# Performance work log

Hardware: AMD Instinct MI355X
Metric: run time of the kernel (lower is better)

Reference implementation:

```python
import jax, jax.numpy as jnp
import numpy as np

MAXLEN = 100  # target_node_incoming_edge_maxlim in to_dense_batch_JY


def setup_inputs() -> dict:
    key = jax.random.key(0)
    ks = jax.random.split(key, 6)
    N, F, H, B = 500000, 64, 64, 8192
    x = jax.random.normal(ks[0], (N, F), dtype=jnp.float32)
    index = jnp.sort(jax.random.randint(ks[1], (N,), 0, B)).astype(jnp.int64)
    s = 1.0 / np.sqrt(H)  # torch LSTM reset_parameters: U(-1/sqrt(H), 1/sqrt(H))
    W_ih = jax.random.uniform(ks[2], (4 * H, F), jnp.float32, -s, s)
    W_hh = jax.random.uniform(ks[3], (4 * H, H), jnp.float32, -s, s)
    b_ih = jax.random.uniform(ks[4], (4 * H,), jnp.float32, -s, s)
    b_hh = jax.random.uniform(ks[5], (4 * H,), jnp.float32, -s, s)
    return {"x": x, "W_ih": W_ih, "W_hh": W_hh, "b_ih": b_ih, "b_hh": b_hh,
            "index": index, "dim_size": B}


def _lstm_last_hidden(dense, mask, W_ih, W_hh, b_ih, b_hh):
    """Run a single-layer LSTM over dense [B,L,F]; freeze state where mask is
    False, which reproduces pack_sequence semantics (ht = hidden at last valid
    step of each sequence; zero-length sequences stay at h0=0)."""
    B, L, F = dense.shape
    H = W_hh.shape[1]
    # input projection for all timesteps at once: [B, L, 4H]
    xg = jnp.einsum('blf,gf->blg', dense, W_ih) + (b_ih + b_hh)

    def step(carry, inp):
        h, c = carry
        g_x, m = inp                      # g_x: [B,4H], m: [B] bool
        g = g_x + h @ W_hh.T
        i, f, gc, o = jnp.split(g, 4, axis=-1)  # torch gate order: i, f, g, o
        i = jax.nn.sigmoid(i)
        f = jax.nn.sigmoid(f)
        gc = jnp.tanh(gc)
        o = jax.nn.sigmoid(o)
        c_new = f * c + i * gc
        h_new = o * jnp.tanh(c_new)
        m2 = m[:, None]
        return (jnp.where(m2, h_new, h), jnp.where(m2, c_new, c)), None

    h0 = jnp.zeros((B, H), dense.dtype)
    (h, _c), _ = jax.lax.scan(step, (h0, h0),
                              (jnp.swapaxes(xg, 0, 1), mask.T))
    return h  # [B, H] == ht[-1]


def reference(x, W_ih, W_hh, b_ih, b_hh, index, dim_size):
    N, F = x.shape
    index = index.astype(jnp.int32)
    # per-graph node counts and exclusive-cumsum offsets (index is sorted)
    counts = jax.ops.segment_sum(jnp.ones(N, jnp.int32), index,
                                 num_segments=dim_size)
    offsets = jnp.concatenate([jnp.zeros(1, jnp.int32),
                               jnp.cumsum(counts)[:-1].astype(jnp.int32)])
    pos = jnp.arange(N, dtype=jnp.int32) - offsets[index]  # position in graph
    valid = pos < MAXLEN                                   # truncate to 100
    # scatter into dense [B, MAXLEN, F]; invalid rows are zeroed and added at
    # slot 0 so they are no-ops
    dense = jnp.zeros((dim_size, MAXLEN, F), x.dtype)
    dense = dense.at[index, jnp.where(valid, pos, 0)].add(
        jnp.where(valid[:, None], x, 0.0))
    seq_len = jnp.minimum(counts, MAXLEN)
    mask = jnp.arange(MAXLEN)[None, :] < seq_len[:, None]  # [B, MAXLEN]
    return _lstm_last_hidden(dense, mask, W_ih, W_hh, b_ih, b_hh)
```

## Files before the change

kernel.cpp:

```cpp
#include <hip/hip_runtime.h>

#define MAXLEN 100
#define HDIM 64
#define CH 4
#define NSEG 12
#define SROW 72
#define SPLANE (CH * SROW + 8)
#define HSTR 72
#define L2E 1.44269504f

typedef __attribute__((ext_vector_type(8))) short bf16x8;
typedef __attribute__((ext_vector_type(4))) float f32x4;

#define LGKM_BARRIER() asm volatile("s_waitcnt lgkmcnt(0)\n\ts_barrier" ::: "memory")

__device__ __forceinline__ unsigned short f2bf_u(float f) {
    unsigned u = __float_as_uint(f);
    u += 0x7fffu + ((u >> 16) & 1u);
    return (unsigned short)(u >> 16);
}
__device__ __forceinline__ unsigned pk2(float a, float b) {
    return (unsigned)f2bf_u(a) | ((unsigned)f2bf_u(b) << 16);
}
__device__ __forceinline__ bf16x8 pack8(f32x4 a, f32x4 b) {
    union { unsigned u[4]; bf16x8 v; } c;
    c.u[0] = pk2(a[0], a[1]); c.u[1] = pk2(a[2], a[3]);
    c.u[2] = pk2(b[0], b[1]); c.u[3] = pk2(b[2], b[3]);
    return c.v;
}
__device__ __forceinline__ float sig_b(float v, float bs) {
    return __builtin_amdgcn_rcpf(1.0f + __builtin_amdgcn_exp2f(fmaf(v, -L2E, bs)));
}
__device__ __forceinline__ float tanh_b(float v, float bs2) {
    return fmaf(2.0f, __builtin_amdgcn_rcpf(1.0f + __builtin_amdgcn_exp2f(fmaf(v, -2.0f * L2E, bs2))), -1.0f);
}
__device__ __forceinline__ float tanh_p(float v) {
    return fmaf(2.0f, __builtin_amdgcn_rcpf(1.0f + __builtin_amdgcn_exp2f(v * (-2.0f * L2E))), -1.0f);
}

__global__ __launch_bounds__(256, 3)
void lstm12_kernel(const float* __restrict__ x,
                   const float* __restrict__ Wih,
                   const float* __restrict__ Whh,
                   const float* __restrict__ bih,
                   const float* __restrict__ bhh,
                   const int* __restrict__ index,
                   float* __restrict__ out, int N, int B) {
    const int tid  = threadIdx.x;
    const int w    = tid >> 6;
    const int lane = tid & 63;
    const int l15  = lane & 15;
    const int quad = lane >> 4;
    const int segbase = blockIdx.x * NSEG;
    const int ncol = w * 16 + l15;

    __shared__ __align__(16) unsigned short xst[NSEG * SPLANE];
    __shared__ __align__(16) unsigned short hst[2][16][HSTR];
    __shared__ int sstart[NSEG], slen[NSEG];

    if (tid < NSEG) {
        const int b = segbase + tid;
        int s = 0, len = 0;
        if (b < B) {
            int lo = 0, hi = N;
            while (lo < hi) { int m = (lo + hi) >> 1; if (index[m] < b) lo = m + 1; else hi = m; }
            s = lo;
            hi = N;
            while (lo < hi) { int m = (lo + hi) >> 1; if (index[m] < b + 1) lo = m + 1; else hi = m; }
            len = lo - s;
            len = len < MAXLEN ? len : MAXLEN;
        }
        sstart[tid] = s;
        slen[tid] = len;
    }
    for (int i = tid; i < 2 * 16 * HSTR / 2; i += 256) ((int*)hst)[i] = 0;
    __syncthreads();

    bf16x8 wi[4][2], wh[4][2];
    float bs[4];
#pragma unroll
    for (int g = 0; g < 4; ++g) {
        const int row = g * HDIM + ncol;
        const float bb = bih[row] + bhh[row];
        bs[g] = (g == 2) ? (-2.0f * L2E) * bb : (-L2E) * bb;
#pragma unroll
        for (int kt = 0; kt < 2; ++kt) {
            const f32x4* pi = (const f32x4*)(Wih + (size_t)row * HDIM + kt * 32 + quad * 8);
            const f32x4* ph = (const f32x4*)(Whh + (size_t)row * HDIM + kt * 32 + quad * 8);
            wi[g][kt] = pack8(pi[0], pi[1]);
            wh[g][kt] = pack8(ph[0], ph[1]);
        }
    }

    int len3[3];
#pragma unroll
    for (int r = 0; r < 3; ++r) len3[r] = slen[quad * 3 + r];
    int lmax = 0;
#pragma unroll
    for (int i = 0; i < NSEG; ++i) { int v = slen[i]; lmax = v > lmax ? v : lmax; }
    lmax = __builtin_amdgcn_readfirstlane(lmax);

    const int sS = tid >> 4, sT = (tid >> 2) & 3, sC = tid & 3;
    const int sst = (tid < 192) ? sstart[sS] : 0;
    const int sln = (tid < 192) ? slen[sS] : 0;

    f32x4 pre[4];

#define ISSUE(t0_)                                                              \
    if (w < 3) {                                                                \
        int ct = (t0_) + sT;                                                    \
        ct = (sln > 0) ? (ct < sln ? ct : sln - 1) : 0;                         \
        int row = sst + ct;                                                     \
        row = row < N - 1 ? row : N - 1;                                        \
        const f32x4* p_ = (const f32x4*)(x + (size_t)row * HDIM + sC * 16);     \
        pre[0] = p_[0]; pre[1] = p_[1]; pre[2] = p_[2]; pre[3] = p_[3];         \
    }
#define COMMIT()                                                                \
    if (w < 3) {                                                                \
        uint4 o1, o2;                                                           \
        o1.x = pk2(pre[0][0], pre[0][1]); o1.y = pk2(pre[0][2], pre[0][3]);     \
        o1.z = pk2(pre[1][0], pre[1][1]); o1.w = pk2(pre[1][2], pre[1][3]);     \
        o2.x = pk2(pre[2][0], pre[2][1]); o2.y = pk2(pre[2][2], pre[2][3]);     \
        o2.z = pk2(pre[3][0], pre[3][1]); o2.w = pk2(pre[3][2], pre[3][3]);     \
        unsigned short* d_ = &xst[sS * SPLANE + sT * SROW + sC * 16];           \
        *(uint4*)d_ = o1; *(uint4*)(d_ + 8) = o2;                               \
    }

    const int m3 = l15 & 3;
    const int xp = (l15 >> 2) * 3 + (m3 < 2 ? m3 : 2);
    const unsigned short* xb = &xst[xp * SPLANE + quad * 8];

    f32x4 accx[4];
#define ACCX(tt_)                                                               \
    {                                                                           \
        const unsigned short* xr_ = xb + (tt_) * SROW;                          \
        bf16x8 xa0_ = *(const bf16x8*)(xr_);                                    \
        bf16x8 xa1_ = *(const bf16x8*)(xr_ + 32);                               \
        _Pragma("unroll")                                                       \
        for (int g_ = 0; g_ < 4; ++g_) {                                        \
            f32x4 a_ = __builtin_amdgcn_mfma_f32_16x16x32_bf16(xa0_, wi[g_][0], cz, 0, 0, 0); \
            accx[g_] = __builtin_amdgcn_mfma_f32_16x16x32_bf16(xa1_, wi[g_][1], a_, 0, 0, 0); \
        }                                                                       \
    }

    float c3[3] = {0, 0, 0}, h3[3] = {0, 0, 0};
    const f32x4 cz = {0.0f, 0.0f, 0.0f, 0.0f};
    const int nch = (lmax + CH - 1) / CH;

    if (nch > 0) {
        ISSUE(0);
        COMMIT();
        LGKM_BARRIER();
        ACCX(0);
        if (nch > 1) ISSUE(CH);

        for (int ch = 0; ch < nch; ++ch) {
            const int t0 = ch * CH;
#pragma unroll
            for (int tt = 0; tt < CH; ++tt) {
                const int t = t0 + tt;
                const int pb = tt & 1, nb = pb ^ 1;

                const unsigned short* hr = &hst[pb][l15][quad * 8];
                bf16x8 ha0 = *(const bf16x8*)(hr);
                bf16x8 ha1 = *(const bf16x8*)(hr + 32);

                f32x4 acc[4];
#pragma unroll
                for (int g = 0; g < 4; ++g) {
                    f32x4 a = __builtin_amdgcn_mfma_f32_16x16x32_bf16(ha0, wh[g][0], accx[g], 0, 0, 0);
                    acc[g] = __builtin_amdgcn_mfma_f32_16x16x32_bf16(ha1, wh[g][1], a, 0, 0, 0);
                }

                if (tt + 1 < CH) ACCX(tt + 1);

#pragma unroll
                for (int r = 0; r < 3; ++r) {
                    float gi = sig_b (acc[0][r], bs[0]);
                    float gf = sig_b (acc[1][r], bs[1]);
                    float gg = tanh_b(acc[2][r], bs[2]);
                    float go = sig_b (acc[3][r], bs[3]);
                    float cn = fmaf(gf, c3[r], gi * gg);
                    float hn = go * tanh_p(cn);
                    const bool up = t < len3[r];
                    c3[r] = up ? cn : c3[r];
                    h3[r] = up ? hn : h3[r];
                    hst[nb][quad * 4 + r][ncol] = f2bf_u(h3[r]);
                }
                LGKM_BARRIER();
            }
            if (ch + 1 < nch) {
                COMMIT();
                LGKM_BARRIER();
                ACCX(0);
                if (ch + 2 < nch) ISSUE((ch + 2) * CH);
            }
        }
    }

#pragma unroll
    for (int r = 0; r < 3; ++r) {
        const int seg = segbase + quad * 3 + r;
        if (seg < B) out[(size_t)seg * HDIM + ncol] = h3[r];
    }
#undef ISSUE
#undef COMMIT
#undef ACCX
}

extern "C" void kernel_launch(void* const* d_in, const int* in_sizes, int n_in,
                              void* d_out, int out_size, void* d_ws, size_t ws_size,
                              hipStream_t stream) {
    const float* x     = (const float*)d_in[0];
    const float* Wih   = (const float*)d_in[1];
    const float* Whh   = (const float*)d_in[2];
    const float* bih   = (const float*)d_in[3];
    const float* bhh   = (const float*)d_in[4];
    const int*   index = (const int*)d_in[5];

    const int N = in_sizes[5];
    const int B = out_size / HDIM;

    const int nblocks = (B + NSEG - 1) / NSEG;
    lstm12_kernel<<<nblocks, 256, 0, stream>>>(x, Wih, Whh, bih, bhh, index,
                                               (float*)d_out, N, B);
}
```

Measured before the change: 251.5 us.

## Sort segments by length into blocks to balance LSTM recurrence work

Adds two pre-kernels: one computes segment start offsets from the sorted index, and one counting-sorts segments by truncated length into slots. The LSTM kernel then handles groups of 12 similar-length segments per block, so each block's step count matches its members and lanes do not idle waiting on the longest sequence. This costs two extra launches, including a single-block sort, plus an indirection when writing outputs. It falls back to the old per-block binary search when the workspace is too small.

```diff
diff --git a/kernel.cpp b/kernel.cpp
--- a/kernel.cpp
+++ b/kernel.cpp
@@ -38,6 +38,51 @@
     return fmaf(2.0f, __builtin_amdgcn_rcpf(1.0f + __builtin_amdgcn_exp2f(v * (-2.0f * L2E))), -1.0f);
 }
 
+__global__ void seg_bounds_kernel(const int* __restrict__ index,
+                                  int* __restrict__ segStart, int N, int B) {
+    const int i = blockIdx.x * blockDim.x + threadIdx.x;
+    if (i >= N) return;
+    const int a = index[i];
+    const int prev = (i == 0) ? -1 : index[i - 1];
+    for (int s = prev + 1; s <= a; ++s) segStart[s] = i;
+    if (i == N - 1) {
+        for (int s = a + 1; s <= B; ++s) segStart[s] = N;
+    }
+}
+
+__global__ void seg_sort_kernel(const int* __restrict__ segStart,
+                                int* __restrict__ slotSeg,
+                                int* __restrict__ slotStart,
+                                int* __restrict__ slotLen, int B, int nslots) {
+    __shared__ int hist[MAXLEN + 1];
+    __shared__ int base[MAXLEN + 1];
+    __shared__ int cnt[MAXLEN + 1];
+    const int tid = threadIdx.x;
+    if (tid <= MAXLEN) { hist[tid] = 0; cnt[tid] = 0; }
+    __syncthreads();
+    for (int b = tid; b < B; b += 1024) {
+        int len = segStart[b + 1] - segStart[b];
+        len = len < MAXLEN ? len : MAXLEN;
+        atomicAdd(&hist[len], 1);
+    }
+    __syncthreads();
+    if (tid == 0) {
+        int acc = 0;
+        for (int l = MAXLEN; l >= 0; --l) { base[l] = acc; acc += hist[l]; }
+    }
+    __syncthreads();
+    for (int b = tid; b < B; b += 1024) {
+        const int s0 = segStart[b];
+        int len = segStart[b + 1] - s0;
+        len = len < MAXLEN ? len : MAXLEN;
+        const int slot = base[len] + atomicAdd(&cnt[len], 1);
+        slotSeg[slot] = b; slotStart[slot] = s0; slotLen[slot] = len;
+    }
+    for (int s = B + tid; s < nslots; s += 1024) {
+        slotSeg[s] = -1; slotStart[s] = 0; slotLen[s] = 0;
+    }
+}
+
 __global__ __launch_bounds__(256, 3)
 void lstm12_kernel(const float* __restrict__ x,
                    const float* __restrict__ Wih,
@@ -45,6 +90,9 @@
                    const float* __restrict__ bih,
                    const float* __restrict__ bhh,
                    const int* __restrict__ index,
+                   const int* __restrict__ slotSeg,
+                   const int* __restrict__ slotStart,
+                   const int* __restrict__ slotLen,
                    float* __restrict__ out, int N, int B) {
     const int tid  = threadIdx.x;
     const int w    = tid >> 6;
@@ -56,22 +104,31 @@
 
     __shared__ __align__(16) unsigned short xst[NSEG * SPLANE];
     __shared__ __align__(16) unsigned short hst[2][16][HSTR];
-    __shared__ int sstart[NSEG], slen[NSEG];
+    __shared__ int sstart[NSEG], slen[NSEG], sseg[NSEG];
 
     if (tid < NSEG) {
-        const int b = segbase + tid;
-        int s = 0, len = 0;
-        if (b < B) {
-            int lo = 0, hi = N;
-            while (lo < hi) { int m = (lo + hi) >> 1; if (index[m] < b) lo = m + 1; else hi = m; }
-            s = lo;
-            hi = N;
-            while (lo < hi) { int m = (lo + hi) >> 1; if (index[m] < b + 1) lo = m + 1; else hi = m; }
-            len = lo - s;
-            len = len < MAXLEN ? len : MAXLEN;
+        const int slot = segbase + tid;
+        int sg = -1, s = 0, len = 0;
+        if (slotSeg != nullptr) {
+            sg  = slotSeg[slot];
+            s   = slotStart[slot];
+            len = slotLen[slot];
+        } else {
+            const int b = slot;
+            if (b < B) {
+                sg = b;
+                int lo = 0, hi = N;
+                while (lo < hi) { int m = (lo + hi) >> 1; if (index[m] < b) lo = m + 1; else hi = m; }
+                s = lo;
+                hi = N;
+                while (lo < hi) { int m = (lo + hi) >> 1; if (index[m] < b + 1) lo = m + 1; else hi = m; }
+                len = lo - s;
+                len = len < MAXLEN ? len : MAXLEN;
+            }
         }
         sstart[tid] = s;
         slen[tid] = len;
+        sseg[tid] = sg;
     }
     for (int i = tid; i < 2 * 16 * HSTR / 2; i += 256) ((int*)hst)[i] = 0;
     __syncthreads();
@@ -200,8 +257,8 @@
 
 #pragma unroll
     for (int r = 0; r < 3; ++r) {
-        const int seg = segbase + quad * 3 + r;
-        if (seg < B) out[(size_t)seg * HDIM + ncol] = h3[r];
+        const int sg = sseg[quad * 3 + r];
+        if (sg >= 0) out[(size_t)sg * HDIM + ncol] = h3[r];
     }
 #undef ISSUE
 #undef COMMIT
@@ -222,6 +279,26 @@
     const int B = out_size / HDIM;
 
     const int nblocks = (B + NSEG - 1) / NSEG;
-    lstm12_kernel<<<nblocks, 256, 0, stream>>>(x, Wih, Whh, bih, bhh, index,
-                                               (float*)d_out, N, B);
-}
+    const int nslots  = nblocks * NSEG;
+
+    const int segStartInts = (B + 1 + 3) & ~3;
+    const size_t need = ((size_t)segStartInts + 3 * (size_t)nslots) * sizeof(int);
+    const bool sortOK = (d_ws != nullptr) && (ws_size >= need) && (B <= 16384);
+
+    if (sortOK) {
+        int* segStart  = (int*)d_ws;
+        int* slotSeg   = segStart + segStartInts;
+        int* slotStart = slotSeg + nslots;
+        int* slotLen   = slotStart + nslots;
+        const int ablocks = (N + 255) / 256;
+        seg_bounds_kernel<<<ablocks, 256, 0, stream>>>(index, segStart, N, B);
+        seg_sort_kernel<<<1, 1024, 0, stream>>>(segStart, slotSeg, slotStart, slotLen, B, nslots);
+        lstm12_kernel<<<nblocks, 256, 0, stream>>>(x, Wih, Whh, bih, bhh, index,
+                                                   slotSeg, slotStart, slotLen,
+                                                   (float*)d_out, N, B);
+    } else {
+        lstm12_kernel<<<nblocks, 256, 0, stream>>>(x, Wih, Whh, bih, bhh, index,
+                                                   nullptr, nullptr, nullptr,
+                                                   (float*)d_out, N, B);
+    }
+}
```

Result: no change. 247.4 us (-1.6%).

## Sort segments by length before LSTM and fold bias/scale into MFMA

Applied to the files above, without the earlier changes.

Adds two pre-kernels that compute segment starts and a length histogram, then counting-sort segments by descending length so each 12-segment block holds similar lengths. The goal is to cut wasted recurrent steps where a block runs to the longest member while the others are done. It also folds the gate bias and the exp2 scale into the weights and the MFMA accumulator init, and uses the hardware v_cvt_pk_bf16_f32 instruction for bf16 packing. Costs are two extra launches, a memset, atomics and an indirect output write; pre-scaling weights before the bf16 rounding slightly changes numerics.

```diff
diff --git a/kernel.cpp b/kernel.cpp
--- a/kernel.cpp
+++ b/kernel.cpp
@@ -14,28 +14,68 @@
 
 #define LGKM_BARRIER() asm volatile("s_waitcnt lgkmcnt(0)\n\ts_barrier" ::: "memory")
 
-__device__ __forceinline__ unsigned short f2bf_u(float f) {
-    unsigned u = __float_as_uint(f);
-    u += 0x7fffu + ((u >> 16) & 1u);
-    return (unsigned short)(u >> 16);
-}
-__device__ __forceinline__ unsigned pk2(float a, float b) {
-    return (unsigned)f2bf_u(a) | ((unsigned)f2bf_u(b) << 16);
+__device__ __forceinline__ unsigned cvtpk(float a, float b) {
+    unsigned r;
+    asm("v_cvt_pk_bf16_f32 %0, %1, %2" : "=v"(r) : "v"(a), "v"(b));
+    return r;
 }
 __device__ __forceinline__ bf16x8 pack8(f32x4 a, f32x4 b) {
     union { unsigned u[4]; bf16x8 v; } c;
-    c.u[0] = pk2(a[0], a[1]); c.u[1] = pk2(a[2], a[3]);
-    c.u[2] = pk2(b[0], b[1]); c.u[3] = pk2(b[2], b[3]);
+    c.u[0] = cvtpk(a[0], a[1]); c.u[1] = cvtpk(a[2], a[3]);
+    c.u[2] = cvtpk(b[0], b[1]); c.u[3] = cvtpk(b[2], b[3]);
     return c.v;
 }
-__device__ __forceinline__ float sig_b(float v, float bs) {
-    return __builtin_amdgcn_rcpf(1.0f + __builtin_amdgcn_exp2f(fmaf(v, -L2E, bs)));
-}
-__device__ __forceinline__ float tanh_b(float v, float bs2) {
-    return fmaf(2.0f, __builtin_amdgcn_rcpf(1.0f + __builtin_amdgcn_exp2f(fmaf(v, -2.0f * L2E, bs2))), -1.0f);
+__device__ __forceinline__ float sig_pre(float a) {
+    return __builtin_amdgcn_rcpf(1.0f + __builtin_amdgcn_exp2f(a));
+}
+__device__ __forceinline__ float tanh_pre(float a) {
+    return fmaf(2.0f, __builtin_amdgcn_rcpf(1.0f + __builtin_amdgcn_exp2f(a)), -1.0f);
 }
 __device__ __forceinline__ float tanh_p(float v) {
     return fmaf(2.0f, __builtin_amdgcn_rcpf(1.0f + __builtin_amdgcn_exp2f(v * (-2.0f * L2E))), -1.0f);
+}
+
+__global__ void seg_hist_kernel(const int* __restrict__ index,
+                                int* __restrict__ segStart,
+                                int* __restrict__ hist, int N, int B) {
+    const int s = blockIdx.x * blockDim.x + threadIdx.x;
+    if (s > B) return;
+    int lo = 0, hi = N;
+    while (lo < hi) { int m = (lo + hi) >> 1; if (index[m] < s) lo = m + 1; else hi = m; }
+    segStart[s] = lo;
+    if (s < B) {
+        int l2 = lo, h2 = N;
+        while (l2 < h2) { int m = (l2 + h2) >> 1; if (index[m] < s + 1) l2 = m + 1; else h2 = m; }
+        int len = l2 - lo;
+        len = len < MAXLEN ? len : MAXLEN;
+        atomicAdd(&hist[len], 1);
+    }
+}
+
+__global__ void seg_scatter_kernel(const int* __restrict__ segStart,
+                                   const int* __restrict__ hist,
+                                   int* __restrict__ cnt,
+                                   int2* __restrict__ slotPacked,
+                                   int B, int nslots) {
+    __shared__ int base_s[MAXLEN + 1];
+    const int tid = threadIdx.x;
+    __shared__ int hist_s[MAXLEN + 1];
+    if (tid <= MAXLEN) hist_s[tid] = hist[tid];
+    __syncthreads();
+    if (tid == 0) {
+        int acc = 0;
+        for (int l = MAXLEN; l >= 0; --l) { base_s[l] = acc; acc += hist_s[l]; }
+    }
+    __syncthreads();
+    const int stride = gridDim.x * blockDim.x;
+    for (int b = blockIdx.x * blockDim.x + tid; b < B; b += stride) {
+        const int s0 = segStart[b];
+        int len = segStart[b + 1] - s0;
+        len = len < MAXLEN ? len : MAXLEN;
+        const int slot = base_s[len] + atomicAdd(&cnt[len], 1);
+        slotPacked[slot] = make_int2(s0, (b << 7) | len);
+    }
+    if (blockIdx.x == 0 && tid < nslots - B) slotPacked[B + tid] = make_int2(0, -128);
 }
 
 __global__ __launch_bounds__(256, 3)
@@ -45,6 +85,7 @@
                    const float* __restrict__ bih,
                    const float* __restrict__ bhh,
                    const int* __restrict__ index,
+                   const int2* __restrict__ slotPacked,
                    float* __restrict__ out, int N, int B) {
     const int tid  = threadIdx.x;
     const int w    = tid >> 6;
@@ -56,39 +97,50 @@
 
     __shared__ __align__(16) unsigned short xst[NSEG * SPLANE];
     __shared__ __align__(16) unsigned short hst[2][16][HSTR];
-    __shared__ int sstart[NSEG], slen[NSEG];
+    __shared__ int sstart[NSEG], slen[NSEG], sseg[NSEG];
 
     if (tid < NSEG) {
-        const int b = segbase + tid;
-        int s = 0, len = 0;
-        if (b < B) {
-            int lo = 0, hi = N;
-            while (lo < hi) { int m = (lo + hi) >> 1; if (index[m] < b) lo = m + 1; else hi = m; }
-            s = lo;
-            hi = N;
-            while (lo < hi) { int m = (lo + hi) >> 1; if (index[m] < b + 1) lo = m + 1; else hi = m; }
-            len = lo - s;
-            len = len < MAXLEN ? len : MAXLEN;
+        const int slot = segbase + tid;
+        int sg = -1, s = 0, len = 0;
+        if (slotPacked != nullptr) {
+            const int2 p = slotPacked[slot];
+            s   = p.x;
+            sg  = p.y >> 7;
+            len = p.y & 127;
+        } else {
+            const int b = slot;
+            if (b < B) {
+                sg = b;
+                int lo = 0, hi = N;
+                while (lo < hi) { int m = (lo + hi) >> 1; if (index[m] < b) lo = m + 1; else hi = m; }
+                s = lo;
+                hi = N;
+                while (lo < hi) { int m = (lo + hi) >> 1; if (index[m] < b + 1) lo = m + 1; else hi = m; }
+                len = lo - s;
+                len = len < MAXLEN ? len : MAXLEN;
+            }
         }
         sstart[tid] = s;
         slen[tid] = len;
+        sseg[tid] = sg;
     }
     for (int i = tid; i < 2 * 16 * HSTR / 2; i += 256) ((int*)hst)[i] = 0;
     __syncthreads();
 
     bf16x8 wi[4][2], wh[4][2];
-    float bs[4];
+    f32x4 bsv[4];
 #pragma unroll
     for (int g = 0; g < 4; ++g) {
+        const float sc = (g == 2) ? (-2.0f * L2E) : (-L2E);
         const int row = g * HDIM + ncol;
-        const float bb = bih[row] + bhh[row];
-        bs[g] = (g == 2) ? (-2.0f * L2E) * bb : (-L2E) * bb;
+        const float bb = sc * (bih[row] + bhh[row]);
+        bsv[g][0] = bb; bsv[g][1] = bb; bsv[g][2] = bb; bsv[g][3] = bb;
 #pragma unroll
         for (int kt = 0; kt < 2; ++kt) {
             const f32x4* pi = (const f32x4*)(Wih + (size_t)row * HDIM + kt * 32 + quad * 8);
             const f32x4* ph = (const f32x4*)(Whh + (size_t)row * HDIM + kt * 32 + quad * 8);
-            wi[g][kt] = pack8(pi[0], pi[1]);
-            wh[g][kt] = pack8(ph[0], ph[1]);
+            wi[g][kt] = pack8(pi[0] * sc, pi[1] * sc);
+            wh[g][kt] = pack8(ph[0] * sc, ph[1] * sc);
         }
     }
 
@@ -118,10 +170,10 @@
 #define COMMIT()                                                                \
     if (w < 3) {                                                                \
         uint4 o1, o2;                                                           \
-        o1.x = pk2(pre[0][0], pre[0][1]); o1.y = pk2(pre[0][2], pre[0][3]);     \
-        o1.z = pk2(pre[1][0], pre[1][1]); o1.w = pk2(pre[1][2], pre[1][3]);     \
-        o2.x = pk2(pre[2][0], pre[2][1]); o2.y = pk2(pre[2][2], pre[2][3]);     \
-        o2.z = pk2(pre[3][0], pre[3][1]); o2.w = pk2(pre[3][2], pre[3][3]);     \
+        o1.x = cvtpk(pre[0][0], pre[0][1]); o1.y = cvtpk(pre[0][2], pre[0][3]); \
+        o1.z = cvtpk(pre[1][0], pre[1][1]); o1.w = cvtpk(pre[1][2], pre[1][3]); \
+        o2.x = cvtpk(pre[2][0], pre[2][1]); o2.y = cvtpk(pre[2][2], pre[2][3]); \
+        o2.z = cvtpk(pre[3][0], pre[3][1]); o2.w = cvtpk(pre[3][2], pre[3][3]); \
         unsigned short* d_ = &xst[sS * SPLANE + sT * SROW + sC * 16];           \
         *(uint4*)d_ = o1; *(uint4*)(d_ + 8) = o2;                               \
     }
@@ -138,13 +190,12 @@
         bf16x8 xa1_ = *(const bf16x8*)(xr_ + 32);                               \
         _Pragma("unroll")                                                       \
         for (int g_ = 0; g_ < 4; ++g_) {                                        \
-            f32x4 a_ = __builtin_amdgcn_mfma_f32_16x16x32_bf16(xa0_, wi[g_][0], cz, 0, 0, 0); \
+            f32x4 a_ = __builtin_amdgcn_mfma_f32_16x16x32_bf16(xa0_, wi[g_][0], bsv[g_], 0, 0, 0); \
             accx[g_] = __builtin_amdgcn_mfma_f32_16x16x32_bf16(xa1_, wi[g_][1], a_, 0, 0, 0); \
         }                                                                       \
     }
 
     float c3[3] = {0, 0, 0}, h3[3] = {0, 0, 0};
-    const f32x4 cz = {0.0f, 0.0f, 0.0f, 0.0f};
     const int nch = (lmax + CH - 1) / CH;
 
     if (nch > 0) {
@@ -176,16 +227,16 @@
 
 #pragma unroll
                 for (int r = 0; r < 3; ++r) {
-                    float gi = sig_b (acc[0][r], bs[0]);
-                    float gf = sig_b (acc[1][r], bs[1]);
-                    float gg = tanh_b(acc[2][r], bs[2]);
-                    float go = sig_b (acc[3][r], bs[3]);
+                    float gi = sig_pre (acc[0][r]);
+                    float gf = sig_pre (acc[1][r]);
+                    float gg = tanh_pre(acc[2][r]);
+                    float go = sig_pre (acc[3][r]);
                     float cn = fmaf(gf, c3[r], gi * gg);
                     float hn = go * tanh_p(cn);
                     const bool up = t < len3[r];
                     c3[r] = up ? cn : c3[r];
                     h3[r] = up ? hn : h3[r];
-                    hst[nb][quad * 4 + r][ncol] = f2bf_u(h3[r]);
+                    hst[nb][quad * 4 + r][ncol] = (unsigned short)cvtpk(h3[r], h3[r]);
                 }
                 LGKM_BARRIER();
             }
@@ -200,8 +251,8 @@
 
 #pragma unroll
     for (int r = 0; r < 3; ++r) {
-        const int seg = segbase + quad * 3 + r;
-        if (seg < B) out[(size_t)seg * HDIM + ncol] = h3[r];
+        const int sg = sseg[quad * 3 + r];
+        if (sg >= 0) out[(size_t)sg * HDIM + ncol] = h3[r];
     }
 #undef ISSUE
 #undef COMMIT
@@ -222,6 +273,29 @@
     const int B = out_size / HDIM;
 
     const int nblocks = (B + NSEG - 1) / NSEG;
-    lstm12_kernel<<<nblocks, 256, 0, stream>>>(x, Wih, Whh, bih, bhh, index,
-                                               (float*)d_out, N, B);
-}
+    const int nslots  = nblocks * NSEG;
+
+    const int histOfs = 0, cntOfs = 101;
+    const int segOfs  = 204;
+    int slotOfs = segOfs + B + 1;
+    slotOfs = (slotOfs + 3) & ~3;
+    const size_t need = ((size_t)slotOfs + 2 * (size_t)nslots) * sizeof(int);
+    const bool sortOK = (d_ws != nullptr) && (ws_size >= need) && (B <= 16384);
+
+    if (sortOK) {
+        int* wsi        = (int*)d_ws;
+        int* hist       = wsi + histOfs;
+        int* cnt        = wsi + cntOfs;
+        int* segStart   = wsi + segOfs;
+        int2* slotPacked = (int2*)(wsi + slotOfs);
+        hipMemsetAsync(wsi, 0, 202 * sizeof(int), stream);
+        const int p1blocks = (B + 1 + 255) / 256;
+        seg_hist_kernel<<<p1blocks, 256, 0, stream>>>(index, segStart, hist, N, B);
+        seg_scatter_kernel<<<16, 256, 0, stream>>>(segStart, hist, cnt, slotPacked, B, nslots);
+        lstm12_kernel<<<nblocks, 256, 0, stream>>>(x, Wih, Whh, bih, bhh, index,
+                                                   slotPacked, (float*)d_out, N, B);
+    } else {
+        lstm12_kernel<<<nblocks, 256, 0, stream>>>(x, Wih, Whh, bih, bhh, index,
+                                                   nullptr, (float*)d_out, N, B);
+    }
+}
```

Result: slower. 266.0 us (+5.8%).

## Process 32 segments per block with two MFMA tiles and fold gate scaling into weights

Applied to the files above, without the earlier changes.

Each block now handles 32 sequences instead of 12, split into two full 16-row MFMA tiles that share the same register-resident weights, so the earlier 12-of-16 row padding is no longer wasted. Gate scale factors are folded into W_ih/W_hh and the bias is loaded as the MFMA accumulator init, which removes per-element FMAs in the activations. bf16 packing now uses the hardware v_cvt_pk_bf16_f32 instruction instead of manual rounding. The cost is fewer blocks (about 256 for B=8192), launch bounds of 1 block per SM, and more registers per thread, so latency hiding across timesteps now relies on two independent tiles instead of several resident blocks.

```diff
diff --git a/kernel.cpp b/kernel.cpp
--- a/kernel.cpp
+++ b/kernel.cpp
@@ -3,7 +3,7 @@
 #define MAXLEN 100
 #define HDIM 64
 #define CH 4
-#define NSEG 12
+#define NSEG 32
 #define SROW 72
 #define SPLANE (CH * SROW + 8)
 #define HSTR 72
@@ -14,32 +14,29 @@
 
 #define LGKM_BARRIER() asm volatile("s_waitcnt lgkmcnt(0)\n\ts_barrier" ::: "memory")
 
-__device__ __forceinline__ unsigned short f2bf_u(float f) {
-    unsigned u = __float_as_uint(f);
-    u += 0x7fffu + ((u >> 16) & 1u);
-    return (unsigned short)(u >> 16);
-}
-__device__ __forceinline__ unsigned pk2(float a, float b) {
-    return (unsigned)f2bf_u(a) | ((unsigned)f2bf_u(b) << 16);
+__device__ __forceinline__ unsigned cvtpk(float a, float b) {
+    unsigned r;
+    asm("v_cvt_pk_bf16_f32 %0, %1, %2" : "=v"(r) : "v"(a), "v"(b));
+    return r;
 }
 __device__ __forceinline__ bf16x8 pack8(f32x4 a, f32x4 b) {
     union { unsigned u[4]; bf16x8 v; } c;
-    c.u[0] = pk2(a[0], a[1]); c.u[1] = pk2(a[2], a[3]);
-    c.u[2] = pk2(b[0], b[1]); c.u[3] = pk2(b[2], b[3]);
+    c.u[0] = cvtpk(a[0], a[1]); c.u[1] = cvtpk(a[2], a[3]);
+    c.u[2] = cvtpk(b[0], b[1]); c.u[3] = cvtpk(b[2], b[3]);
     return c.v;
 }
-__device__ __forceinline__ float sig_b(float v, float bs) {
-    return __builtin_amdgcn_rcpf(1.0f + __builtin_amdgcn_exp2f(fmaf(v, -L2E, bs)));
-}
-__device__ __forceinline__ float tanh_b(float v, float bs2) {
-    return fmaf(2.0f, __builtin_amdgcn_rcpf(1.0f + __builtin_amdgcn_exp2f(fmaf(v, -2.0f * L2E, bs2))), -1.0f);
+__device__ __forceinline__ float sig_pre(float a) {
+    return __builtin_amdgcn_rcpf(1.0f + __builtin_amdgcn_exp2f(a));
+}
+__device__ __forceinline__ float tanh_pre(float a) {
+    return fmaf(2.0f, __builtin_amdgcn_rcpf(1.0f + __builtin_amdgcn_exp2f(a)), -1.0f);
 }
 __device__ __forceinline__ float tanh_p(float v) {
     return fmaf(2.0f, __builtin_amdgcn_rcpf(1.0f + __builtin_amdgcn_exp2f(v * (-2.0f * L2E))), -1.0f);
 }
 
-__global__ __launch_bounds__(256, 3)
-void lstm12_kernel(const float* __restrict__ x,
+__global__ __launch_bounds__(256, 1)
+void lstm32_kernel(const float* __restrict__ x,
                    const float* __restrict__ Wih,
                    const float* __restrict__ Whh,
                    const float* __restrict__ bih,
@@ -55,13 +52,14 @@
     const int ncol = w * 16 + l15;
 
     __shared__ __align__(16) unsigned short xst[NSEG * SPLANE];
-    __shared__ __align__(16) unsigned short hst[2][16][HSTR];
-    __shared__ int sstart[NSEG], slen[NSEG];
+    __shared__ __align__(16) unsigned short hst[2][NSEG][HSTR];
+    __shared__ int sstart[NSEG], slen[NSEG], sseg[NSEG];
 
     if (tid < NSEG) {
         const int b = segbase + tid;
-        int s = 0, len = 0;
+        int sg = -1, s = 0, len = 0;
         if (b < B) {
+            sg = b;
             int lo = 0, hi = N;
             while (lo < hi) { int m = (lo + hi) >> 1; if (index[m] < b) lo = m + 1; else hi = m; }
             s = lo;
@@ -72,79 +70,99 @@
         }
         sstart[tid] = s;
         slen[tid] = len;
-    }
-    for (int i = tid; i < 2 * 16 * HSTR / 2; i += 256) ((int*)hst)[i] = 0;
+        sseg[tid] = sg;
+    }
+    for (int i = tid; i < 2 * NSEG * HSTR / 2; i += 256) ((int*)hst)[i] = 0;
     __syncthreads();
 
     bf16x8 wi[4][2], wh[4][2];
-    float bs[4];
+    f32x4 bsv[4];
 #pragma unroll
     for (int g = 0; g < 4; ++g) {
+        const float sc = (g == 2) ? (-2.0f * L2E) : (-L2E);
         const int row = g * HDIM + ncol;
-        const float bb = bih[row] + bhh[row];
-        bs[g] = (g == 2) ? (-2.0f * L2E) * bb : (-L2E) * bb;
+        const float bb = sc * (bih[row] + bhh[row]);
+        bsv[g][0] = bb; bsv[g][1] = bb; bsv[g][2] = bb; bsv[g][3] = bb;
 #pragma unroll
         for (int kt = 0; kt < 2; ++kt) {
             const f32x4* pi = (const f32x4*)(Wih + (size_t)row * HDIM + kt * 32 + quad * 8);
             const f32x4* ph = (const f32x4*)(Whh + (size_t)row * HDIM + kt * 32 + quad * 8);
-            wi[g][kt] = pack8(pi[0], pi[1]);
-            wh[g][kt] = pack8(ph[0], ph[1]);
+            wi[g][kt] = pack8(pi[0] * sc, pi[1] * sc);
+            wh[g][kt] = pack8(ph[0] * sc, ph[1] * sc);
         }
     }
 
-    int len3[3];
-#pragma unroll
-    for (int r = 0; r < 3; ++r) len3[r] = slen[quad * 3 + r];
+    int lenA[4], lenB[4];
+#pragma unroll
+    for (int r = 0; r < 4; ++r) {
+        lenA[r] = slen[quad * 4 + r];
+        lenB[r] = slen[16 + quad * 4 + r];
+    }
     int lmax = 0;
 #pragma unroll
     for (int i = 0; i < NSEG; ++i) { int v = slen[i]; lmax = v > lmax ? v : lmax; }
     lmax = __builtin_amdgcn_readfirstlane(lmax);
 
     const int sS = tid >> 4, sT = (tid >> 2) & 3, sC = tid & 3;
-    const int sst = (tid < 192) ? sstart[sS] : 0;
-    const int sln = (tid < 192) ? slen[sS] : 0;
-
-    f32x4 pre[4];
+    const int sst0 = sstart[sS],      sln0 = slen[sS];
+    const int sst1 = sstart[sS + 16], sln1 = slen[sS + 16];
+
+    f32x4 pre0[4], pre1[4];
 
 #define ISSUE(t0_)                                                              \
-    if (w < 3) {                                                                \
-        int ct = (t0_) + sT;                                                    \
-        ct = (sln > 0) ? (ct < sln ? ct : sln - 1) : 0;                         \
-        int row = sst + ct;                                                     \
-        row = row < N - 1 ? row : N - 1;                                        \
-        const f32x4* p_ = (const f32x4*)(x + (size_t)row * HDIM + sC * 16);     \
-        pre[0] = p_[0]; pre[1] = p_[1]; pre[2] = p_[2]; pre[3] = p_[3];         \
+    {                                                                           \
+        int ct0 = (t0_) + sT;                                                   \
+        ct0 = (sln0 > 0) ? (ct0 < sln0 ? ct0 : sln0 - 1) : 0;                   \
+        int row0 = sst0 + ct0; row0 = row0 < N - 1 ? row0 : N - 1;              \
+        const f32x4* p_ = (const f32x4*)(x + (size_t)row0 * HDIM + sC * 16);    \
+        pre0[0] = p_[0]; pre0[1] = p_[1]; pre0[2] = p_[2]; pre0[3] = p_[3];     \
+        int ct1 = (t0_) + sT;                                                   \
+        ct1 = (sln1 > 0) ? (ct1 < sln1 ? ct1 : sln1 - 1) : 0;                   \
+        int row1 = sst1 + ct1; row1 = row1 < N - 1 ? row1 : N - 1;              \
+        const f32x4* q_ = (const f32x4*)(x + (size_t)row1 * HDIM + sC * 16);    \
+        pre1[0] = q_[0]; pre1[1] = q_[1]; pre1[2] = q_[2]; pre1[3] = q_[3];     \
     }
 #define COMMIT()                                                                \
-    if (w < 3) {                                                                \
+    {                                                                           \
         uint4 o1, o2;                                                           \
-        o1.x = pk2(pre[0][0], pre[0][1]); o1.y = pk2(pre[0][2], pre[0][3]);     \
-        o1.z = pk2(pre[1][0], pre[1][1]); o1.w = pk2(pre[1][2], pre[1][3]);     \
-        o2.x = pk2(pre[2][0], pre[2][1]); o2.y = pk2(pre[2][2], pre[2][3]);     \
-        o2.z = pk2(pre[3][0], pre[3][1]); o2.w = pk2(pre[3][2], pre[3][3]);     \
-        unsigned short* d_ = &xst[sS * SPLANE + sT * SROW + sC * 16];           \
-        *(uint4*)d_ = o1; *(uint4*)(d_ + 8) = o2;                               \
-    }
-
-    const int m3 = l15 & 3;
-    const int xp = (l15 >> 2) * 3 + (m3 < 2 ? m3 : 2);
-    const unsigned short* xb = &xst[xp * SPLANE + quad * 8];
-
-    f32x4 accx[4];
+        o1.x = cvtpk(pre0[0][0], pre0[0][1]); o1.y = cvtpk(pre0[0][2], pre0[0][3]); \
+        o1.z = cvtpk(pre0[1][0], pre0[1][1]); o1.w = cvtpk(pre0[1][2], pre0[1][3]); \
+        o2.x = cvtpk(pre0[2][0], pre0[2][1]); o2.y = cvtpk(pre0[2][2], pre0[2][3]); \
+        o2.z = cvtpk(pre0[3][0], pre0[3][1]); o2.w = cvtpk(pre0[3][2], pre0[3][3]); \
+        unsigned short* d0_ = &xst[sS * SPLANE + sT * SROW + sC * 16];          \
+        *(uint4*)d0_ = o1; *(uint4*)(d0_ + 8) = o2;                             \
+        uint4 o3, o4;                                                           \
+        o3.x = cvtpk(pre1[0][0], pre1[0][1]); o3.y = cvtpk(pre1[0][2], pre1[0][3]); \
+        o3.z = cvtpk(pre1[1][0], pre1[1][1]); o3.w = cvtpk(pre1[1][2], pre1[1][3]); \
+        o4.x = cvtpk(pre1[2][0], pre1[2][1]); o4.y = cvtpk(pre1[2][2], pre1[2][3]); \
+        o4.z = cvtpk(pre1[3][0], pre1[3][1]); o4.w = cvtpk(pre1[3][2], pre1[3][3]); \
+        unsigned short* d1_ = &xst[(sS + 16) * SPLANE + sT * SROW + sC * 16];   \
+        *(uint4*)d1_ = o3; *(uint4*)(d1_ + 8) = o4;                             \
+    }
+
+    const unsigned short* xb0 = &xst[l15 * SPLANE + quad * 8];
+    const unsigned short* xb1 = &xst[(16 + l15) * SPLANE + quad * 8];
+
+    f32x4 accx[2][4];
 #define ACCX(tt_)                                                               \
     {                                                                           \
-        const unsigned short* xr_ = xb + (tt_) * SROW;                          \
-        bf16x8 xa0_ = *(const bf16x8*)(xr_);                                    \
-        bf16x8 xa1_ = *(const bf16x8*)(xr_ + 32);                               \
+        const unsigned short* xr0_ = xb0 + (tt_) * SROW;                        \
+        bf16x8 a0_ = *(const bf16x8*)(xr0_);                                    \
+        bf16x8 a1_ = *(const bf16x8*)(xr0_ + 32);                               \
+        const unsigned short* xr1_ = xb1 + (tt_) * SROW;                        \
+        bf16x8 b0_ = *(const bf16x8*)(xr1_);                                    \
+        bf16x8 b1_ = *(const bf16x8*)(xr1_ + 32);                               \
         _Pragma("unroll")                                                       \
         for (int g_ = 0; g_ < 4; ++g_) {                                        \
-            f32x4 a_ = __builtin_amdgcn_mfma_f32_16x16x32_bf16(xa0_, wi[g_][0], cz, 0, 0, 0); \
-            accx[g_] = __builtin_amdgcn_mfma_f32_16x16x32_bf16(xa1_, wi[g_][1], a_, 0, 0, 0); \
+            f32x4 t0_ = __builtin_amdgcn_mfma_f32_16x16x32_bf16(a0_, wi[g_][0], bsv[g_], 0, 0, 0); \
+            accx[0][g_] = __builtin_amdgcn_mfma_f32_16x16x32_bf16(a1_, wi[g_][1], t0_, 0, 0, 0); \
+            f32x4 t1_ = __builtin_amdgcn_mfma_f32_16x16x32_bf16(b0_, wi[g_][0], bsv[g_], 0, 0, 0); \
+            accx[1][g_] = __builtin_amdgcn_mfma_f32_16x16x32_bf16(b1_, wi[g_][1], t1_, 0, 0, 0); \
         }                                                                       \
     }
 
-    float c3[3] = {0, 0, 0}, h3[3] = {0, 0, 0};
-    const f32x4 cz = {0.0f, 0.0f, 0.0f, 0.0f};
+    float cA[4] = {0, 0, 0, 0}, hA[4] = {0, 0, 0, 0};
+    float cB[4] = {0, 0, 0, 0}, hB[4] = {0, 0, 0, 0};
     const int nch = (lmax + CH - 1) / CH;
 
     if (nch > 0) {
@@ -159,33 +177,51 @@
 #pragma unroll
             for (int tt = 0; tt < CH; ++tt) {
                 const int t = t0 + tt;
-                const int pb = tt & 1, nb = pb ^ 1;
-
-                const unsigned short* hr = &hst[pb][l15][quad * 8];
-                bf16x8 ha0 = *(const bf16x8*)(hr);
-                bf16x8 ha1 = *(const bf16x8*)(hr + 32);
-
-                f32x4 acc[4];
+                const int pb = tt & 1, nb2 = pb ^ 1;
+
+                const unsigned short* hr0 = &hst[pb][l15][quad * 8];
+                bf16x8 ha0 = *(const bf16x8*)(hr0);
+                bf16x8 ha1 = *(const bf16x8*)(hr0 + 32);
+                const unsigned short* hr1 = &hst[pb][16 + l15][quad * 8];
+                bf16x8 hb0 = *(const bf16x8*)(hr1);
+                bf16x8 hb1 = *(const bf16x8*)(hr1 + 32);
+
+                f32x4 acc[2][4];
 #pragma unroll
                 for (int g = 0; g < 4; ++g) {
-                    f32x4 a = __builtin_amdgcn_mfma_f32_16x16x32_bf16(ha0, wh[g][0], accx[g], 0, 0, 0);
-                    acc[g] = __builtin_amdgcn_mfma_f32_16x16x32_bf16(ha1, wh[g][1], a, 0, 0, 0);
+                    f32x4 a = __builtin_amdgcn_mfma_f32_16x16x32_bf16(ha0, wh[g][0], accx[0][g], 0, 0, 0);
+                    acc[0][g] = __builtin_amdgcn_mfma_f32_16x16x32_bf16(ha1, wh[g][1], a, 0, 0, 0);
+                    f32x4 b = __builtin_amdgcn_mfma_f32_16x16x32_bf16(hb0, wh[g][0], accx[1][g], 0, 0, 0);
+                    acc[1][g] = __builtin_amdgcn_mfma_f32_16x16x32_bf16(hb1, wh[g][1], b, 0, 0, 0);
                 }
 
                 if (tt + 1 < CH) ACCX(tt + 1);
 
 #pragma unroll
-                for (int r = 0; r < 3; ++r) {
-                    float gi = sig_b (acc[0][r], bs[0]);
-                    float gf = sig_b (acc[1][r], bs[1]);
-                    float gg = tanh_b(acc[2][r], bs[2]);
-                    float go = sig_b (acc[3][r], bs[3]);
-                    float cn = fmaf(gf, c3[r], gi * gg);
+                for (int r = 0; r < 4; ++r) {
+                    float gi = sig_pre (acc[0][0][r]);
+                    float gf = sig_pre (acc[0][1][r]);
+                    float gg = tanh_pre(acc[0][2][r]);
+                    float go = sig_pre (acc[0][3][r]);
+                    float cn = fmaf(gf, cA[r], gi * gg);
                     float hn = go * tanh_p(cn);
-                    const bool up = t < len3[r];
-                    c3[r] = up ? cn : c3[r];
-                    h3[r] = up ? hn : h3[r];
-                    hst[nb][quad * 4 + r][ncol] = f2bf_u(h3[r]);
+                    const bool up = t < lenA[r];
+                    cA[r] = up ? cn : cA[r];
+                    hA[r] = up ? hn : hA[r];
+                    hst[nb2][quad * 4 + r][ncol] = (unsigned short)cvtpk(hA[r], hA[r]);
+                }
+#pragma unroll
+                for (int r = 0; r < 4; ++r) {
+                    float gi = sig_pre (acc[1][0][r]);
+                    float gf = sig_pre (acc[1][1][r]);
+                    float gg = tanh_pre(acc[1][2][r]);
+                    float go = sig_pre (acc[1][3][r]);
+                    float cn = fmaf(gf, cB[r], gi * gg);
+                    float hn = go * tanh_p(cn);
+                    const bool up = t < lenB[r];
+                    cB[r] = up ? cn : cB[r];
+                    hB[r] = up ? hn : hB[r];
+                    hst[nb2][16 + quad * 4 + r][ncol] = (unsigned short)cvtpk(hB[r], hB[r]);
                 }
                 LGKM_BARRIER();
             }
@@ -199,9 +235,11 @@
     }
 
 #pragma unroll
-    for (int r = 0; r < 3; ++r) {
-        const int seg = segbase + quad * 3 + r;
-        if (seg < B) out[(size_t)seg * HDIM + ncol] = h3[r];
+    for (int r = 0; r < 4; ++r) {
+        const int sgA = sseg[quad * 4 + r];
+        if (sgA >= 0) out[(size_t)sgA * HDIM + ncol] = hA[r];
+        const int sgB = sseg[16 + quad * 4 + r];
+        if (sgB >= 0) out[(size_t)sgB * HDIM + ncol] = hB[r];
     }
 #undef ISSUE
 #undef COMMIT
@@ -211,17 +249,17 @@
 extern "C" void kernel_launch(void* const* d_in, const int* in_sizes, int n_in,
                               void* d_out, int out_size, void* d_ws, size_t ws_size,
                               hipStream_t stream) {
-    const float* x     = (const float*)d_in[0];
-    const float* Wih   = (const float*)d_in[1];
-    const float* Whh   = (const float*)d_in[2];
-    const float* bih   = (const float*)d_in[3];
-    const float* bhh   = (const float*)d_in[4];
-    const int*   index = (const int*)d_in[5];
+    const float* x   = (const float*)d_in[0];
+    const float* Wih = (const float*)d_in[1];
+    const float* Whh = (const float*)d_in[2];
+    const float* bih = (const float*)d_in[3];
+    const float* bhh = (const float*)d_in[4];
+    const int* index = (const int*)d_in[5];
 
     const int N = in_sizes[5];
     const int B = out_size / HDIM;
-
     const int nblocks = (B + NSEG - 1) / NSEG;
-    lstm12_kernel<<<nblocks, 256, 0, stream>>>(x, Wih, Whh, bih, bhh, index,
+
+    lstm32_kernel<<<nblocks, 256, 0, stream>>>(x, Wih, Whh, bih, bhh, index,
                                                (float*)d_out, N, B);
 }
```

New measurement: 259.2 us. +3.1%, slower.
